# Kernel tuning notes

Hardware: AMD Instinct MI355X
Metric: run time of the kernel (lower is better)

The kernel has to match this reference:

```python
import jax, jax.numpy as jnp
import numpy as np

N_NODES = 100000
N_EDGES = 1600000
BN_EPS = 1e-5

def gin_layer(h, src, dst, eps, w1, b1, w2, b2, gamma, beta, mean, var):
    # message passing: sum of source-node features at each target node
    agg = jax.ops.segment_sum(h[src], dst, num_segments=h.shape[0])  # [N, H]
    z = (1.0 + eps) * h + agg
    z = jax.nn.relu(z @ w1 + b1)
    z = jax.nn.relu(z @ w2 + b2)
    # BatchNorm1d in eval mode (running stats as params)
    return gamma * (z - mean) * jax.lax.rsqrt(var + BN_EPS) + beta

def setup_inputs() -> dict:
    key = jax.random.key(0)
    ks = jax.random.split(key, 12)
    H = 64
    s = lambda fan: 1.0 / np.sqrt(fan)
    inp = {
        "x": jax.random.normal(ks[0], (N_NODES, 128), jnp.float32),
        "edge_index": jax.random.randint(ks[1], (2, N_EDGES), 0, N_NODES, jnp.int64),
        "eps": jnp.zeros((3,), jnp.float32),
        "c1_w1": jax.random.normal(ks[2], (128, H), jnp.float32) * s(128),
        "c1_b1": jnp.zeros((H,), jnp.float32),
        "c1_w2": jax.random.normal(ks[3], (H, H), jnp.float32) * s(H),
        "c1_b2": jnp.zeros((H,), jnp.float32),
        "c1_gamma": jnp.ones((H,), jnp.float32),
        "c1_beta": jnp.zeros((H,), jnp.float32),
        "c1_mean": jnp.zeros((H,), jnp.float32),
        "c1_var": jnp.ones((H,), jnp.float32),
        "cw1": jax.random.normal(ks[4], (2, H, H), jnp.float32) * s(H),
        "cb1": jnp.zeros((2, H), jnp.float32),
        "cw2": jax.random.normal(ks[5], (2, H, H), jnp.float32) * s(H),
        "cb2": jnp.zeros((2, H), jnp.float32),
        "cgamma": jnp.ones((2, H), jnp.float32),
        "cbeta": jnp.zeros((2, H), jnp.float32),
        "cmean": jnp.zeros((2, H), jnp.float32),
        "cvar": jnp.ones((2, H), jnp.float32),
        "lin1_w": jax.random.normal(ks[6], (H, H), jnp.float32) * s(H),
        "lin1_b": jnp.zeros((H,), jnp.float32),
        "lin2_w": jax.random.normal(ks[7], (H, 40), jnp.float32) * s(H),
        "lin2_b": jnp.zeros((40,), jnp.float32),
    }
    return inp

def reference(x, edge_index, eps, c1_w1, c1_b1, c1_w2, c1_b2, c1_gamma, c1_beta,
              c1_mean, c1_var, cw1, cb1, cw2, cb2, cgamma, cbeta, cmean, cvar,
              lin1_w, lin1_b, lin2_w, lin2_b):
    src, dst = edge_index[0], edge_index[1]
    h = gin_layer(x, src, dst, eps[0], c1_w1, c1_b1, c1_w2, c1_b2,
                  c1_gamma, c1_beta, c1_mean, c1_var)
    for i in range(2):  # num_layers - 1 stacked GINConvs
        h = gin_layer(h, src, dst, eps[i + 1], cw1[i], cb1[i], cw2[i], cb2[i],
                      cgamma[i], cbeta[i], cmean[i], cvar[i])
    h = jax.nn.relu(h @ lin1_w + lin1_b)
    # dropout(p=0.5) is identity in eval mode
    return h @ lin2_w + lin2_b  # logits [N, num_classes]
```

## Files before the change

kernel.cpp:

```cpp
#include <hip/hip_runtime.h>

#define NN 100000
#define NE 1600000
#define BN_EPS 1e-5f
#define NCOARSE 98
#define SC_CH 2048

typedef unsigned int u32;
typedef unsigned short u16;

static constexpr size_t OFF_ROW  = 0;
static constexpr size_t OFF_CTRL = 512u * 1024;
static constexpr size_t OFF_CSR  = 1u << 20;
static constexpr size_t OFF_U    = 8u << 20;
static constexpr size_t OFF_P1   = OFF_U;
static constexpr size_t OFF_YB0  = OFF_U + (size_t)NN * 64 * 4;
static constexpr size_t OFF_YB1  = OFF_YB0 + (size_t)NN * 64 * 2;

__device__ __forceinline__ u16 f2bf(float f) {
  u32 u = __float_as_uint(f);
  return (u16)((u + 0x7fffu + ((u >> 16) & 1u)) >> 16);
}
__device__ __forceinline__ float bflo(u32 u) { return __uint_as_float(u << 16); }
__device__ __forceinline__ float bfhi(u32 u) { return __uint_as_float(u & 0xffff0000u); }
__device__ __forceinline__ u32 pkbf(float lo, float hi) {
  return (u32)f2bf(lo) | ((u32)f2bf(hi) << 16);
}

typedef __bf16 bf16x8 __attribute__((ext_vector_type(8)));
typedef float f32x4 __attribute__((ext_vector_type(4)));
union FragCvt { uint4 u; bf16x8 b; u16 s[8]; };
__device__ __forceinline__ bf16x8 frag_u16(const u16* p) {
  FragCvt c; c.u = *(const uint4*)p; return c.b;
}

__global__ void __launch_bounds__(256) k_hist_c(const int* __restrict__ dst,
                                                int* __restrict__ ch) {
  __shared__ int h[NCOARSE];
  if (threadIdx.x < NCOARSE) h[threadIdx.x] = 0;
  __syncthreads();
  int i = blockIdx.x * 256 + threadIdx.x, stride = gridDim.x * 256;
  for (; i < NE; i += stride) atomicAdd(&h[dst[i] >> 10], 1);
  __syncthreads();
  if (threadIdx.x < NCOARSE && h[threadIdx.x]) atomicAdd(&ch[threadIdx.x], h[threadIdx.x]);
}

__global__ void __launch_bounds__(256) k_scat1(const int* __restrict__ src,
                                               const int* __restrict__ dst,
                                               const int* __restrict__ ch,
                                               int* __restrict__ reserve,
                                               u32* __restrict__ pairs1) {
  __shared__ int coffL[NCOARSE];
  __shared__ int h[NCOARSE], base[NCOARSE];
  int t = threadIdx.x;
  if (t < NCOARSE) { h[t] = 0; coffL[t] = ch[t]; }
  __syncthreads();
  if (t == 0) {
    int acc = 0;
    for (int i = 0; i < NCOARSE; i++) { int v = coffL[i]; coffL[i] = acc; acc += v; }
  }
  int e0 = blockIdx.x * SC_CH;
  int myc[8]; u32 mypk[8];
#pragma unroll
  for (int q = 0; q < 8; q++) {
    int e = e0 + q * 256 + t;
    if (e < NE) {
      int d = dst[e], s = src[e];
      myc[q] = d >> 10;
      mypk[q] = (u32)s | ((u32)(d & 1023) << 17);
      atomicAdd(&h[myc[q]], 1);
    } else myc[q] = -1;
  }
  __syncthreads();
  if (t < NCOARSE) {
    base[t] = (h[t] > 0) ? (coffL[t] + atomicAdd(&reserve[t], h[t])) : 0;
    h[t] = 0;
  }
  __syncthreads();
#pragma unroll
  for (int q = 0; q < 8; q++) {
    if (myc[q] >= 0) {
      int p = atomicAdd(&h[myc[q]], 1);
      pairs1[base[myc[q]] + p] = mypk[q];
    }
  }
}

__global__ void __launch_bounds__(256) k_fill3(const u32* __restrict__ pairs1,
                                               const int* __restrict__ ch,
                                               int* __restrict__ row,
                                               int* __restrict__ csr) {
  __shared__ int coffL[NCOARSE + 1];
  __shared__ int lcnt[1024];
  __shared__ int loff[1024];
  __shared__ int sd[256];
  __shared__ u32 stage[20480];
  int c = blockIdx.x, t = threadIdx.x;
  if (t < NCOARSE) coffL[t] = ch[t];
  __syncthreads();
  if (t == 0) {
    int acc = 0;
    for (int i = 0; i < NCOARSE; i++) { int v = coffL[i]; coffL[i] = acc; acc += v; }
    coffL[NCOARSE] = acc;
  }
  for (int i = t; i < 1024; i += 256) lcnt[i] = 0;
  __syncthreads();
  int es = coffL[c], ee = coffL[c + 1];
  int m = ee - es;
  int nbase = c << 10;
  int nodes_in = NN - nbase; if (nodes_in > 1024) nodes_in = 1024;
  for (int i = es + t; i < ee; i += 256)
    atomicAdd(&lcnt[(pairs1[i] >> 17) & 1023], 1);
  __syncthreads();
  int b4 = t * 4;
  int c0 = lcnt[b4], c1 = lcnt[b4 + 1], c2 = lcnt[b4 + 2], c3 = lcnt[b4 + 3];
  int s4 = c0 + c1 + c2 + c3;
  sd[t] = s4;
  __syncthreads();
  for (int o = 1; o < 256; o <<= 1) {
    int x = (t >= o) ? sd[t - o] : 0;
    __syncthreads();
    sd[t] += x;
    __syncthreads();
  }
  int run = sd[t] - s4;
  loff[b4] = run;     run += c0;
  loff[b4 + 1] = run; run += c1;
  loff[b4 + 2] = run; run += c2;
  loff[b4 + 3] = run;
  __syncthreads();
  for (int i = t; i < nodes_in; i += 256) row[nbase + i] = es + loff[i];
  if (c == NCOARSE - 1 && t == 0) row[NN] = NE;
  for (int i = t; i < 1024; i += 256) lcnt[i] = loff[i];
  __syncthreads();
  if (m <= 20480) {
    for (int i = es + t; i < ee; i += 256) {
      u32 pk = pairs1[i];
      int p = atomicAdd(&lcnt[(pk >> 17) & 1023], 1);
      stage[p] = pk & 0x1FFFFu;
    }
    __syncthreads();
    for (int i = t; i < m; i += 256) csr[es + i] = (int)stage[i];
  } else {
    for (int i = es + t; i < ee; i += 256) {
      u32 pk = pairs1[i];
      int p = atomicAdd(&lcnt[(pk >> 17) & 1023], 1);
      csr[es + p] = (int)(pk & 0x1FFFFu);
    }
  }
}

__global__ void __launch_bounds__(256) k_gemm_x_mfma(const float* __restrict__ x,
                                                     const float* __restrict__ w,
                                                     u16* __restrict__ yb) {
  __shared__ __align__(16) u16 wT[64][136];
  __shared__ __align__(16) u16 ht[4][32][72];
  int tid = threadIdx.x;
  for (int idx = tid; idx < 8192; idx += 256) {
    int k = idx >> 6, n = idx & 63;
    wT[n][k] = f2bf(w[idx]);
  }
  __syncthreads();
  int wid = tid >> 6, lane = tid & 63;
  int grp = blockIdx.x * 4 + wid;
  if (grp >= NN / 32) return;
  int g0 = grp * 32;
  int mrow = lane & 15;
  int kc8 = (lane >> 4) * 8;
  int q4 = (lane >> 4) * 4;
  bf16x8 a[2][4];
#pragma unroll
  for (int mt = 0; mt < 2; mt++) {
    const float* xr = x + (size_t)(g0 + mt * 16 + mrow) * 128;
#pragma unroll
    for (int kc = 0; kc < 4; kc++) {
      float4 v0 = *(const float4*)(xr + kc * 32 + kc8);
      float4 v1 = *(const float4*)(xr + kc * 32 + kc8 + 4);
      FragCvt fc;
      fc.s[0] = f2bf(v0.x); fc.s[1] = f2bf(v0.y); fc.s[2] = f2bf(v0.z); fc.s[3] = f2bf(v0.w);
      fc.s[4] = f2bf(v1.x); fc.s[5] = f2bf(v1.y); fc.s[6] = f2bf(v1.z); fc.s[7] = f2bf(v1.w);
      a[mt][kc] = fc.b;
    }
  }
  f32x4 zero = {0.f, 0.f, 0.f, 0.f};
  f32x4 acc[2][4];
#pragma unroll
  for (int nt = 0; nt < 4; nt++) {
    bf16x8 bf[4];
#pragma unroll
    for (int kc = 0; kc < 4; kc++)
      bf[kc] = frag_u16(&wT[nt * 16 + mrow][kc * 32 + kc8]);
#pragma unroll
    for (int mt = 0; mt < 2; mt++) {
      f32x4 c = __builtin_amdgcn_mfma_f32_16x16x32_bf16(a[mt][0], bf[0], zero, 0, 0, 0);
      c = __builtin_amdgcn_mfma_f32_16x16x32_bf16(a[mt][1], bf[1], c, 0, 0, 0);
      c = __builtin_amdgcn_mfma_f32_16x16x32_bf16(a[mt][2], bf[2], c, 0, 0, 0);
      c = __builtin_amdgcn_mfma_f32_16x16x32_bf16(a[mt][3], bf[3], c, 0, 0, 0);
      acc[mt][nt] = c;
    }
  }
#pragma unroll
  for (int mt = 0; mt < 2; mt++)
#pragma unroll
    for (int nt = 0; nt < 4; nt++)
#pragma unroll
      for (int r = 0; r < 4; r++)
        ht[wid][mt * 16 + q4 + r][nt * 16 + mrow] = f2bf(acc[mt][nt][r]);
  asm volatile("s_waitcnt lgkmcnt(0)" ::: "memory");
#pragma unroll
  for (int it = 0; it < 4; it++) {
    int idx = it * 64 + lane;
    int rw = idx >> 3, ch2 = idx & 7;
    uint4 v = *(const uint4*)&ht[wid][rw][ch2 * 8];
    *(uint4*)(yb + (size_t)(g0 + rw) * 64 + ch2 * 8) = v;
  }
}

__global__ void __launch_bounds__(256) k_agg(
    const u16* __restrict__ yb, const int* __restrict__ row, const int* __restrict__ csr,
    const float* __restrict__ epsv, int ei, const float* __restrict__ b1,
    u16* __restrict__ ub) {
  int t = blockIdx.x * 256 + threadIdx.x;
  int n = t >> 3, g = t & 7;
  if (n >= NN) return;
  const u16* bp = yb + g * 8;
  float a0 = 0, a1 = 0, a2 = 0, a3 = 0, a4 = 0, a5 = 0, a6 = 0, a7 = 0;
  int rs = row[n], re = row[n + 1];
  int i = rs;
  int headEnd = rs + ((4 - (rs & 3)) & 3);
  if (headEnd > re) headEnd = re;
  for (; i < headEnd; ++i) {
    int s = csr[i];
    uint4 v0 = *(const uint4*)(bp + (size_t)s * 64);
    a0 += bflo(v0.x); a1 += bfhi(v0.x); a2 += bflo(v0.y); a3 += bfhi(v0.y);
    a4 += bflo(v0.z); a5 += bfhi(v0.z); a6 += bflo(v0.w); a7 += bfhi(v0.w);
  }
  for (; i + 8 <= re; i += 8) {
    int4 c0 = *(const int4*)(csr + i);
    int4 c1 = *(const int4*)(csr + i + 4);
    int sidx[8] = {c0.x, c0.y, c0.z, c0.w, c1.x, c1.y, c1.z, c1.w};
    uint4 v[8];
#pragma unroll
    for (int q = 0; q < 8; q++)
      v[q] = *(const uint4*)(bp + (size_t)sidx[q] * 64);
#pragma unroll
    for (int q = 0; q < 8; q++) {
      a0 += bflo(v[q].x); a1 += bfhi(v[q].x); a2 += bflo(v[q].y); a3 += bfhi(v[q].y);
      a4 += bflo(v[q].z); a5 += bfhi(v[q].z); a6 += bflo(v[q].w); a7 += bfhi(v[q].w);
    }
  }
  if (i + 4 <= re) {
    int4 c0 = *(const int4*)(csr + i);
    int sidx[4] = {c0.x, c0.y, c0.z, c0.w};
    uint4 v[4];
#pragma unroll
    for (int q = 0; q < 4; q++)
      v[q] = *(const uint4*)(bp + (size_t)sidx[q] * 64);
#pragma unroll
    for (int q = 0; q < 4; q++) {
      a0 += bflo(v[q].x); a1 += bfhi(v[q].x); a2 += bflo(v[q].y); a3 += bfhi(v[q].y);
      a4 += bflo(v[q].z); a5 += bfhi(v[q].z); a6 += bflo(v[q].w); a7 += bfhi(v[q].w);
    }
    i += 4;
  }
  for (; i < re; ++i) {
    int s = csr[i];
    uint4 v0 = *(const uint4*)(bp + (size_t)s * 64);
    a0 += bflo(v0.x); a1 += bfhi(v0.x); a2 += bflo(v0.y); a3 += bfhi(v0.y);
    a4 += bflo(v0.z); a5 += bfhi(v0.z); a6 += bflo(v0.w); a7 += bfhi(v0.w);
  }
  uint4 sv = *(const uint4*)(bp + (size_t)n * 64);
  float e1 = 1.0f + epsv[ei];
  const float* bb = b1 + g * 8;
  float r0 = fmaxf(fmaf(e1, bflo(sv.x), a0 + bb[0]), 0.f);
  float r1 = fmaxf(fmaf(e1, bfhi(sv.x), a1 + bb[1]), 0.f);
  float r2 = fmaxf(fmaf(e1, bflo(sv.y), a2 + bb[2]), 0.f);
  float r3 = fmaxf(fmaf(e1, bfhi(sv.y), a3 + bb[3]), 0.f);
  float r4 = fmaxf(fmaf(e1, bflo(sv.z), a4 + bb[4]), 0.f);
  float r5 = fmaxf(fmaf(e1, bfhi(sv.z), a5 + bb[5]), 0.f);
  float r6 = fmaxf(fmaf(e1, bflo(sv.w), a6 + bb[6]), 0.f);
  float r7 = fmaxf(fmaf(e1, bfhi(sv.w), a7 + bb[7]), 0.f);
  uint4 pk;
  pk.x = pkbf(r0, r1); pk.y = pkbf(r2, r3);
  pk.z = pkbf(r4, r5); pk.w = pkbf(r6, r7);
  *(uint4*)(ub + (size_t)n * 64 + g * 8) = pk;
}

__global__ void __launch_bounds__(256) k_mlp_mfma(
    const u16* __restrict__ ub, const float* __restrict__ w2, const float* __restrict__ b2,
    const float* __restrict__ gamma, const float* __restrict__ beta,
    const float* __restrict__ mean, const float* __restrict__ var,
    const float* __restrict__ wn, u16* __restrict__ yout) {
  __shared__ __align__(16) u16 w2T[64][72];
  __shared__ __align__(16) u16 wnT[64][72];
  __shared__ __align__(16) u16 ht[4][32][72];
  int tid = threadIdx.x;
  for (int idx = tid; idx < 4096; idx += 256) {
    int k = idx >> 6, n = idx & 63;
    w2T[n][k] = f2bf(w2[idx]);
    wnT[n][k] = f2bf(wn[idx]);
  }
  __syncthreads();
  int wid = tid >> 6, lane = tid & 63;
  int grp = blockIdx.x * 4 + wid;
  if (grp >= NN / 32) return;
  int g0 = grp * 32;
  int mrow = lane & 15;
  int kc8 = (lane >> 4) * 8;
  int q4 = (lane >> 4) * 4;
  float bb[4], gl[4], be[4], mn[4], rv[4];
#pragma unroll
  for (int nt = 0; nt < 4; nt++) {
    int j = nt * 16 + mrow;
    bb[nt] = b2[j]; gl[nt] = gamma[j]; be[nt] = beta[j]; mn[nt] = mean[j];
    rv[nt] = rsqrtf(var[j] + BN_EPS);
  }
  bf16x8 a[2][2];
#pragma unroll
  for (int mt = 0; mt < 2; mt++)
#pragma unroll
    for (int kc = 0; kc < 2; kc++)
      a[mt][kc] = frag_u16(ub + (size_t)(g0 + mt * 16 + mrow) * 64 + kc * 32 + kc8);
  f32x4 zero = {0.f, 0.f, 0.f, 0.f};
  f32x4 acc[2][4];
#pragma unroll
  for (int nt = 0; nt < 4; nt++) {
    bf16x8 b0 = frag_u16(&w2T[nt * 16 + mrow][kc8]);
    bf16x8 b1f = frag_u16(&w2T[nt * 16 + mrow][32 + kc8]);
#pragma unroll
    for (int mt = 0; mt < 2; mt++) {
      acc[mt][nt] = __builtin_amdgcn_mfma_f32_16x16x32_bf16(a[mt][0], b0, zero, 0, 0, 0);
      acc[mt][nt] = __builtin_amdgcn_mfma_f32_16x16x32_bf16(a[mt][1], b1f, acc[mt][nt], 0, 0, 0);
    }
  }
#pragma unroll
  for (int mt = 0; mt < 2; mt++)
#pragma unroll
    for (int nt = 0; nt < 4; nt++)
#pragma unroll
      for (int r = 0; r < 4; r++) {
        float v = fmaxf(acc[mt][nt][r] + bb[nt], 0.f);
        float h = fmaf(gl[nt] * (v - mn[nt]), rv[nt], be[nt]);
        ht[wid][mt * 16 + q4 + r][nt * 16 + mrow] = f2bf(h);
      }
  asm volatile("s_waitcnt lgkmcnt(0)" ::: "memory");
  bf16x8 a2[2][2];
#pragma unroll
  for (int mt = 0; mt < 2; mt++)
#pragma unroll
    for (int kc = 0; kc < 2; kc++)
      a2[mt][kc] = frag_u16(&ht[wid][mt * 16 + mrow][kc * 32 + kc8]);
  f32x4 ac2[2][4];
#pragma unroll
  for (int nt = 0; nt < 4; nt++) {
    bf16x8 b0 = frag_u16(&wnT[nt * 16 + mrow][kc8]);
    bf16x8 b1f = frag_u16(&wnT[nt * 16 + mrow][32 + kc8]);
#pragma unroll
    for (int mt = 0; mt < 2; mt++) {
      ac2[mt][nt] = __builtin_amdgcn_mfma_f32_16x16x32_bf16(a2[mt][0], b0, zero, 0, 0, 0);
      ac2[mt][nt] = __builtin_amdgcn_mfma_f32_16x16x32_bf16(a2[mt][1], b1f, ac2[mt][nt], 0, 0, 0);
    }
  }
  asm volatile("s_waitcnt lgkmcnt(0)" ::: "memory");
#pragma unroll
  for (int mt = 0; mt < 2; mt++)
#pragma unroll
    for (int nt = 0; nt < 4; nt++)
#pragma unroll
      for (int r = 0; r < 4; r++)
        ht[wid][mt * 16 + q4 + r][nt * 16 + mrow] = f2bf(ac2[mt][nt][r]);
  asm volatile("s_waitcnt lgkmcnt(0)" ::: "memory");
#pragma unroll
  for (int it = 0; it < 4; it++) {
    int idx = it * 64 + lane;
    int rw = idx >> 3, ch2 = idx & 7;
    uint4 v = *(const uint4*)&ht[wid][rw][ch2 * 8];
    *(uint4*)(yout + (size_t)(g0 + rw) * 64 + ch2 * 8) = v;
  }
}

__global__ void __launch_bounds__(256) k_mlp_final_mfma(
    const u16* __restrict__ ub, const float* __restrict__ w2, const float* __restrict__ b2,
    const float* __restrict__ gamma, const float* __restrict__ beta,
    const float* __restrict__ mean, const float* __restrict__ var,
    const float* __restrict__ l1w, const float* __restrict__ l1b,
    const float* __restrict__ l2w, const float* __restrict__ l2b,
    float* __restrict__ out) {
  __shared__ __align__(16) u16 w2T[64][72];
  __shared__ __align__(16) u16 l1T[64][72];
  __shared__ __align__(16) u16 l2T[48][72];
  __shared__ __align__(16) u16 ht[4][32][72];
  int tid = threadIdx.x;
  for (int idx = tid; idx < 4096; idx += 256) {
    int k = idx >> 6, n = idx & 63;
    w2T[n][k] = f2bf(w2[idx]);
    l1T[n][k] = f2bf(l1w[idx]);
  }
  for (int idx = tid; idx < 3072; idx += 256) {
    int n = idx >> 6, k = idx & 63;
    l2T[n][k] = f2bf((n < 40) ? l2w[k * 40 + n] : 0.f);
  }
  __syncthreads();
  int wid = tid >> 6, lane = tid & 63;
  int grp = blockIdx.x * 4 + wid;
  if (grp >= NN / 32) return;
  int g0 = grp * 32;
  int mrow = lane & 15;
  int kc8 = (lane >> 4) * 8;
  int q4 = (lane >> 4) * 4;
  float bb[4], gl[4], be[4], mn[4], rv[4], l1bv[4];
#pragma unroll
  for (int nt = 0; nt < 4; nt++) {
    int j = nt * 16 + mrow;
    bb[nt] = b2[j]; gl[nt] = gamma[j]; be[nt] = beta[j]; mn[nt] = mean[j];
    rv[nt] = rsqrtf(var[j] + BN_EPS); l1bv[nt] = l1b[j];
  }
  float l2bv[3];
#pragma unroll
  for (int nt = 0; nt < 3; nt++) {
    int j = nt * 16 + mrow;
    l2bv[nt] = (j < 40) ? l2b[j] : 0.f;
  }
  bf16x8 a[2][2];
#pragma unroll
  for (int mt = 0; mt < 2; mt++)
#pragma unroll
    for (int kc = 0; kc < 2; kc++)
      a[mt][kc] = frag_u16(ub + (size_t)(g0 + mt * 16 + mrow) * 64 + kc * 32 + kc8);
  f32x4 zero = {0.f, 0.f, 0.f, 0.f};
  f32x4 acc[2][4];
#pragma unroll
  for (int nt = 0; nt < 4; nt++) {
    bf16x8 b0 = frag_u16(&w2T[nt * 16 + mrow][kc8]);
    bf16x8 b1f = frag_u16(&w2T[nt * 16 + mrow][32 + kc8]);
#pragma unroll
    for (int mt = 0; mt < 2; mt++) {
      acc[mt][nt] = __builtin_amdgcn_mfma_f32_16x16x32_bf16(a[mt][0], b0, zero, 0, 0, 0);
      acc[mt][nt] = __builtin_amdgcn_mfma_f32_16x16x32_bf16(a[mt][1], b1f, acc[mt][nt], 0, 0, 0);
    }
  }
#pragma unroll
  for (int mt = 0; mt < 2; mt++)
#pragma unroll
    for (int nt = 0; nt < 4; nt++)
#pragma unroll
      for (int r = 0; r < 4; r++) {
        float v = fmaxf(acc[mt][nt][r] + bb[nt], 0.f);
        float h = fmaf(gl[nt] * (v - mn[nt]), rv[nt], be[nt]);
        ht[wid][mt * 16 + q4 + r][nt * 16 + mrow] = f2bf(h);
      }
  asm volatile("s_waitcnt lgkmcnt(0)" ::: "memory");
  bf16x8 a2[2][2];
#pragma unroll
  for (int mt = 0; mt < 2; mt++)
#pragma unroll
    for (int kc = 0; kc < 2; kc++)
      a2[mt][kc] = frag_u16(&ht[wid][mt * 16 + mrow][kc * 32 + kc8]);
  f32x4 ac2[2][4];
#pragma unroll
  for (int nt = 0; nt < 4; nt++) {
    bf16x8 b0 = frag_u16(&l1T[nt * 16 + mrow][kc8]);
    bf16x8 b1f = frag_u16(&l1T[nt * 16 + mrow][32 + kc8]);
#pragma unroll
    for (int mt = 0; mt < 2; mt++) {
      ac2[mt][nt] = __builtin_amdgcn_mfma_f32_16x16x32_bf16(a2[mt][0], b0, zero, 0, 0, 0);
      ac2[mt][nt] = __builtin_amdgcn_mfma_f32_16x16x32_bf16(a2[mt][1], b1f, ac2[mt][nt], 0, 0, 0);
    }
  }
  asm volatile("s_waitcnt lgkmcnt(0)" ::: "memory");
#pragma unroll
  for (int mt = 0; mt < 2; mt++)
#pragma unroll
    for (int nt = 0; nt < 4; nt++)
#pragma unroll
      for (int r = 0; r < 4; r++) {
        float f = fmaxf(ac2[mt][nt][r] + l1bv[nt], 0.f);
        ht[wid][mt * 16 + q4 + r][nt * 16 + mrow] = f2bf(f);
      }
  asm volatile("s_waitcnt lgkmcnt(0)" ::: "memory");
  bf16x8 a3[2][2];
#pragma unroll
  for (int mt = 0; mt < 2; mt++)
#pragma unroll
    for (int kc = 0; kc < 2; kc++)
      a3[mt][kc] = frag_u16(&ht[wid][mt * 16 + mrow][kc * 32 + kc8]);
  f32x4 ac3[2][3];
#pragma unroll
  for (int nt = 0; nt < 3; nt++) {
    bf16x8 b0 = frag_u16(&l2T[nt * 16 + mrow][kc8]);
    bf16x8 b1f = frag_u16(&l2T[nt * 16 + mrow][32 + kc8]);
#pragma unroll
    for (int mt = 0; mt < 2; mt++) {
      ac3[mt][nt] = __builtin_amdgcn_mfma_f32_16x16x32_bf16(a3[mt][0], b0, zero, 0, 0, 0);
      ac3[mt][nt] = __builtin_amdgcn_mfma_f32_16x16x32_bf16(a3[mt][1], b1f, ac3[mt][nt], 0, 0, 0);
    }
  }
#pragma unroll
  for (int mt = 0; mt < 2; mt++)
#pragma unroll
    for (int nt = 0; nt < 3; nt++) {
      int j = nt * 16 + mrow;
      if (j < 40) {
#pragma unroll
        for (int r = 0; r < 4; r++)
          out[(size_t)(g0 + mt * 16 + q4 + r) * 40 + j] = ac3[mt][nt][r] + l2bv[nt];
      }
    }
}

extern "C" void kernel_launch(void* const* d_in, const int* in_sizes, int n_in,
                              void* d_out, int out_size, void* d_ws, size_t ws_size,
                              hipStream_t stream) {
  const float* x   = (const float*)d_in[0];
  const int*   ei  = (const int*)d_in[1];
  const int*   src = ei;
  const int*   dst = ei + NE;
  const float* eps = (const float*)d_in[2];
  const float* c1_w1 = (const float*)d_in[3];
  const float* c1_b1 = (const float*)d_in[4];
  const float* c1_w2 = (const float*)d_in[5];
  const float* c1_b2 = (const float*)d_in[6];
  const float* c1_gamma = (const float*)d_in[7];
  const float* c1_beta  = (const float*)d_in[8];
  const float* c1_mean  = (const float*)d_in[9];
  const float* c1_var   = (const float*)d_in[10];
  const float* cw1 = (const float*)d_in[11];
  const float* cb1 = (const float*)d_in[12];
  const float* cw2 = (const float*)d_in[13];
  const float* cb2 = (const float*)d_in[14];
  const float* cgamma = (const float*)d_in[15];
  const float* cbeta  = (const float*)d_in[16];
  const float* cmean  = (const float*)d_in[17];
  const float* cvar   = (const float*)d_in[18];
  const float* lin1_w = (const float*)d_in[19];
  const float* lin1_b = (const float*)d_in[20];
  const float* lin2_w = (const float*)d_in[21];
  const float* lin2_b = (const float*)d_in[22];
  float* out = (float*)d_out;

  char* ws = (char*)d_ws;
  int* row  = (int*)(ws + OFF_ROW);
  int* ctrl = (int*)(ws + OFF_CTRL);
  int* ch      = ctrl;
  int* reserve = ctrl + 128;
  int* csr  = (int*)(ws + OFF_CSR);
  u32* pairs1 = (u32*)(ws + OFF_P1);
  u16* ubuf = (u16*)(ws + OFF_U);
  u16* yb0  = (u16*)(ws + OFF_YB0);
  u16* yb1  = (u16*)(ws + OFF_YB1);

  hipMemsetAsync(ctrl, 0, 256 * 4, stream);

  k_hist_c<<<512, 256, 0, stream>>>(dst, ch);
  k_scat1<<<(NE + SC_CH - 1) / SC_CH, 256, 0, stream>>>(src, dst, ch, reserve, pairs1);
  k_fill3<<<NCOARSE, 256, 0, stream>>>(pairs1, ch, row, csr);

  const int AGG_GRID = (NN * 8) / 256;
  const int MLP_GRID = (NN / 32 + 3) / 4;

  k_gemm_x_mfma<<<MLP_GRID, 256, 0, stream>>>(x, c1_w1, yb0);

  k_agg<<<AGG_GRID, 256, 0, stream>>>(yb0, row, csr, eps, 0, c1_b1, ubuf);
  k_mlp_mfma<<<MLP_GRID, 256, 0, stream>>>(ubuf, c1_w2, c1_b2,
                                           c1_gamma, c1_beta, c1_mean, c1_var,
                                           cw1, yb1);
  k_agg<<<AGG_GRID, 256, 0, stream>>>(yb1, row, csr, eps, 1, cb1, ubuf);
  k_mlp_mfma<<<MLP_GRID, 256, 0, stream>>>(ubuf, cw2, cb2,
                                           cgamma, cbeta, cmean, cvar,
                                           cw1 + 64 * 64, yb0);
  k_agg<<<AGG_GRID, 256, 0, stream>>>(yb0, row, csr, eps, 2, cb1 + 64, ubuf);
  k_mlp_final_mfma<<<MLP_GRID, 256, 0, stream>>>(ubuf, cw2 + 64 * 64, cb2 + 64,
                                                 cgamma + 64, cbeta + 64, cmean + 64, cvar + 64,
                                                 lin1_w, lin1_b, lin2_w, lin2_b,
                                                 out);
}
```

Before: 235.9 us.

## Quantize gathered node features to int8 with per-row scales for aggregation

The GEMM epilogues now quantize each 64-wide output row to int8 with a per-row absmax scale instead of storing bf16. The aggregation kernel gathers the 8-byte int8 chunks plus a float scale per neighbor and dequantizes with FMAs. This halves the bytes moved by the random neighbor gather, which dominates the message-passing kernels. In exchange it adds a scale load per edge, drops the vectorized CSR index loads and the alignment head loop, and loses precision, which may break tolerance checks.

```diff
diff --git a/kernel.cpp b/kernel.cpp
--- a/kernel.cpp
+++ b/kernel.cpp
@@ -8,14 +8,17 @@
 
 typedef unsigned int u32;
 typedef unsigned short u16;
+typedef signed char s8;
 
 static constexpr size_t OFF_ROW  = 0;
 static constexpr size_t OFF_CTRL = 512u * 1024;
 static constexpr size_t OFF_CSR  = 1u << 20;
 static constexpr size_t OFF_U    = 8u << 20;
 static constexpr size_t OFF_P1   = OFF_U;
-static constexpr size_t OFF_YB0  = OFF_U + (size_t)NN * 64 * 4;
-static constexpr size_t OFF_YB1  = OFF_YB0 + (size_t)NN * 64 * 2;
+static constexpr size_t OFF_Q0   = 22u << 20;
+static constexpr size_t OFF_S0   = 30u << 20;
+static constexpr size_t OFF_Q1   = 32u << 20;
+static constexpr size_t OFF_S1   = 40u << 20;
 
 __device__ __forceinline__ u16 f2bf(float f) {
   u32 u = __float_as_uint(f);
@@ -32,6 +35,27 @@
 union FragCvt { uint4 u; bf16x8 b; u16 s[8]; };
 __device__ __forceinline__ bf16x8 frag_u16(const u16* p) {
   FragCvt c; c.u = *(const uint4*)p; return c.b;
+}
+
+__device__ __forceinline__ uint2 q8(uint4 hv, float inv) {
+  float v0 = bflo(hv.x), v1 = bfhi(hv.x), v2 = bflo(hv.y), v3 = bfhi(hv.y);
+  float v4 = bflo(hv.z), v5 = bfhi(hv.z), v6 = bflo(hv.w), v7 = bfhi(hv.w);
+  int q0 = (int)rintf(v0 * inv), q1 = (int)rintf(v1 * inv);
+  int q2 = (int)rintf(v2 * inv), q3 = (int)rintf(v3 * inv);
+  int q4 = (int)rintf(v4 * inv), q5 = (int)rintf(v5 * inv);
+  int q6 = (int)rintf(v6 * inv), q7 = (int)rintf(v7 * inv);
+  uint2 r;
+  r.x = (u32)(q0 & 0xff) | ((u32)(q1 & 0xff) << 8) | ((u32)(q2 & 0xff) << 16) | ((u32)(q3 & 0xff) << 24);
+  r.y = (u32)(q4 & 0xff) | ((u32)(q5 & 0xff) << 8) | ((u32)(q6 & 0xff) << 16) | ((u32)(q7 & 0xff) << 24);
+  return r;
+}
+__device__ __forceinline__ float habs8(uint4 hv) {
+  float m = fabsf(bflo(hv.x));
+  m = fmaxf(m, fabsf(bfhi(hv.x))); m = fmaxf(m, fabsf(bflo(hv.y)));
+  m = fmaxf(m, fabsf(bfhi(hv.y))); m = fmaxf(m, fabsf(bflo(hv.z)));
+  m = fmaxf(m, fabsf(bfhi(hv.z))); m = fmaxf(m, fabsf(bflo(hv.w)));
+  m = fmaxf(m, fabsf(bfhi(hv.w)));
+  return m;
 }
 
 __global__ void __launch_bounds__(256) k_hist_c(const int* __restrict__ dst,
@@ -152,7 +176,8 @@
 
 __global__ void __launch_bounds__(256) k_gemm_x_mfma(const float* __restrict__ x,
                                                      const float* __restrict__ w,
-                                                     u16* __restrict__ yb) {
+                                                     s8* __restrict__ qt,
+                                                     float* __restrict__ scal) {
   __shared__ __align__(16) u16 wT[64][136];
   __shared__ __align__(16) u16 ht[4][32][72];
   int tid = threadIdx.x;
@@ -211,75 +236,93 @@
   for (int it = 0; it < 4; it++) {
     int idx = it * 64 + lane;
     int rw = idx >> 3, ch2 = idx & 7;
-    uint4 v = *(const uint4*)&ht[wid][rw][ch2 * 8];
-    *(uint4*)(yb + (size_t)(g0 + rw) * 64 + ch2 * 8) = v;
+    uint4 hv = *(const uint4*)&ht[wid][rw][ch2 * 8];
+    float m = habs8(hv);
+    m = fmaxf(m, __shfl_xor(m, 1));
+    m = fmaxf(m, __shfl_xor(m, 2));
+    m = fmaxf(m, __shfl_xor(m, 4));
+    float inv = (m > 0.f) ? 127.0f / m : 0.f;
+    uint2 qv = q8(hv, inv);
+    *(uint2*)(qt + (size_t)(g0 + rw) * 64 + ch2 * 8) = qv;
+    if (ch2 == 0) scal[g0 + rw] = m * (1.0f / 127.0f);
   }
 }
 
 __global__ void __launch_bounds__(256) k_agg(
-    const u16* __restrict__ yb, const int* __restrict__ row, const int* __restrict__ csr,
+    const s8* __restrict__ qt, const float* __restrict__ scal,
+    const int* __restrict__ row, const int* __restrict__ csr,
     const float* __restrict__ epsv, int ei, const float* __restrict__ b1,
     u16* __restrict__ ub) {
   int t = blockIdx.x * 256 + threadIdx.x;
   int n = t >> 3, g = t & 7;
   if (n >= NN) return;
-  const u16* bp = yb + g * 8;
+  const s8* bp = qt + g * 8;
   float a0 = 0, a1 = 0, a2 = 0, a3 = 0, a4 = 0, a5 = 0, a6 = 0, a7 = 0;
   int rs = row[n], re = row[n + 1];
   int i = rs;
-  int headEnd = rs + ((4 - (rs & 3)) & 3);
-  if (headEnd > re) headEnd = re;
-  for (; i < headEnd; ++i) {
-    int s = csr[i];
-    uint4 v0 = *(const uint4*)(bp + (size_t)s * 64);
-    a0 += bflo(v0.x); a1 += bfhi(v0.x); a2 += bflo(v0.y); a3 += bfhi(v0.y);
-    a4 += bflo(v0.z); a5 += bfhi(v0.z); a6 += bflo(v0.w); a7 += bfhi(v0.w);
-  }
+#define DQ8(qv, sc) { \
+    a0 = fmaf(sc, (float)(int)(s8)((qv).x), a0); \
+    a1 = fmaf(sc, (float)(int)(s8)((qv).x >> 8), a1); \
+    a2 = fmaf(sc, (float)(int)(s8)((qv).x >> 16), a2); \
+    a3 = fmaf(sc, (float)(int)(s8)((qv).x >> 24), a3); \
+    a4 = fmaf(sc, (float)(int)(s8)((qv).y), a4); \
+    a5 = fmaf(sc, (float)(int)(s8)((qv).y >> 8), a5); \
+    a6 = fmaf(sc, (float)(int)(s8)((qv).y >> 16), a6); \
+    a7 = fmaf(sc, (float)(int)(s8)((qv).y >> 24), a7); }
   for (; i + 8 <= re; i += 8) {
-    int4 c0 = *(const int4*)(csr + i);
-    int4 c1 = *(const int4*)(csr + i + 4);
-    int sidx[8] = {c0.x, c0.y, c0.z, c0.w, c1.x, c1.y, c1.z, c1.w};
-    uint4 v[8];
-#pragma unroll
-    for (int q = 0; q < 8; q++)
-      v[q] = *(const uint4*)(bp + (size_t)sidx[q] * 64);
+    int sidx[8];
+#pragma unroll
+    for (int q = 0; q < 8; q++) sidx[q] = csr[i + q];
+    uint2 v[8]; float sc[8];
 #pragma unroll
     for (int q = 0; q < 8; q++) {
-      a0 += bflo(v[q].x); a1 += bfhi(v[q].x); a2 += bflo(v[q].y); a3 += bfhi(v[q].y);
-      a4 += bflo(v[q].z); a5 += bfhi(v[q].z); a6 += bflo(v[q].w); a7 += bfhi(v[q].w);
-    }
+      v[q] = *(const uint2*)(bp + (size_t)sidx[q] * 64);
+      sc[q] = scal[sidx[q]];
+    }
+#pragma unroll
+    for (int q = 0; q < 8; q++) DQ8(v[q], sc[q]);
   }
   if (i + 4 <= re) {
-    int4 c0 = *(const int4*)(csr + i);
-    int sidx[4] = {c0.x, c0.y, c0.z, c0.w};
-    uint4 v[4];
-#pragma unroll
-    for (int q = 0; q < 4; q++)
-      v[q] = *(const uint4*)(bp + (size_t)sidx[q] * 64);
+    int sidx[4];
+#pragma unroll
+    for (int q = 0; q < 4; q++) sidx[q] = csr[i + q];
+    uint2 v[4]; float sc[4];
 #pragma unroll
     for (int q = 0; q < 4; q++) {
-      a0 += bflo(v[q].x); a1 += bfhi(v[q].x); a2 += bflo(v[q].y); a3 += bfhi(v[q].y);
-      a4 += bflo(v[q].z); a5 += bfhi(v[q].z); a6 += bflo(v[q].w); a7 += bfhi(v[q].w);
-    }
+      v[q] = *(const uint2*)(bp + (size_t)sidx[q] * 64);
+      sc[q] = scal[sidx[q]];
+    }
+#pragma unroll
+    for (int q = 0; q < 4; q++) DQ8(v[q], sc[q]);
     i += 4;
   }
   for (; i < re; ++i) {
     int s = csr[i];
-    uint4 v0 = *(const uint4*)(bp + (size_t)s * 64);
-    a0 += bflo(v0.x); a1 += bfhi(v0.x); a2 += bflo(v0.y); a3 += bfhi(v0.y);
-    a4 += bflo(v0.z); a5 += bfhi(v0.z); a6 += bflo(v0.w); a7 += bfhi(v0.w);
-  }
-  uint4 sv = *(const uint4*)(bp + (size_t)n * 64);
+    uint2 v0 = *(const uint2*)(bp + (size_t)s * 64);
+    float sc = scal[s];
+    DQ8(v0, sc);
+  }
+#undef DQ8
+  uint2 sv = *(const uint2*)(bp + (size_t)n * 64);
+  float ssc = scal[n];
+  float s0 = ssc * (float)(int)(s8)(sv.x);
+  float s1 = ssc * (float)(int)(s8)(sv.x >> 8);
+  float s2 = ssc * (float)(int)(s8)(sv.x >> 16);
+  float s3 = ssc * (float)(int)(s8)(sv.x >> 24);
+  float s4 = ssc * (float)(int)(s8)(sv.y);
+  float s5 = ssc * (float)(int)(s8)(sv.y >> 8);
+  float s6 = ssc * (float)(int)(s8)(sv.y >> 16);
+  float s7 = ssc * (float)(int)(s8)(sv.y >> 24);
   float e1 = 1.0f + epsv[ei];
   const float* bb = b1 + g * 8;
-  float r0 = fmaxf(fmaf(e1, bflo(sv.x), a0 + bb[0]), 0.f);
-  float r1 = fmaxf(fmaf(e1, bfhi(sv.x), a1 + bb[1]), 0.f);
-  float r2 = fmaxf(fmaf(e1, bflo(sv.y), a2 + bb[2]), 0.f);
-  float r3 = fmaxf(fmaf(e1, bfhi(sv.y), a3 + bb[3]), 0.f);
-  float r4 = fmaxf(fmaf(e1, bflo(sv.z), a4 + bb[4]), 0.f);
-  float r5 = fmaxf(fmaf(e1, bfhi(sv.z), a5 + bb[5]), 0.f);
-  float r6 = fmaxf(fmaf(e1, bflo(sv.w), a6 + bb[6]), 0.f);
-  float r7 = fmaxf(fmaf(e1, bfhi(sv.w), a7 + bb[7]), 0.f);
+  float r0 = fmaxf(fmaf(e1, s0, a0 + bb[0]), 0.f);
+  float r1 = fmaxf(fmaf(e1, s1, a1 + bb[1]), 0.f);
+  float r2 = fmaxf(fmaf(e1, s2, a2 + bb[2]), 0.f);
+  float r3 = fmaxf(fmaf(e1, s3, a3 + bb[3]), 0.f);
+  float r4 = fmaxf(fmaf(e1, s4, a4 + bb[4]), 0.f);
+  float r5 = fmaxf(fmaf(e1, s5, a5 + bb[5]), 0.f);
+  float r6 = fmaxf(fmaf(e1, s6, a6 + bb[6]), 0.f);
+  float r7 = fmaxf(fmaf(e1, s7, a7 + bb[7]), 0.f);
   uint4 pk;
   pk.x = pkbf(r0, r1); pk.y = pkbf(r2, r3);
   pk.z = pkbf(r4, r5); pk.w = pkbf(r6, r7);
@@ -290,7 +333,7 @@
     const u16* __restrict__ ub, const float* __restrict__ w2, const float* __restrict__ b2,
     const float* __restrict__ gamma, const float* __restrict__ beta,
     const float* __restrict__ mean, const float* __restrict__ var,
-    const float* __restrict__ wn, u16* __restrict__ yout) {
+    const float* __restrict__ wn, s8* __restrict__ qt, float* __restrict__ scal) {
   __shared__ __align__(16) u16 w2T[64][72];
   __shared__ __align__(16) u16 wnT[64][72];
   __shared__ __align__(16) u16 ht[4][32][72];
@@ -374,8 +417,15 @@
   for (int it = 0; it < 4; it++) {
     int idx = it * 64 + lane;
     int rw = idx >> 3, ch2 = idx & 7;
-    uint4 v = *(const uint4*)&ht[wid][rw][ch2 * 8];
-    *(uint4*)(yout + (size_t)(g0 + rw) * 64 + ch2 * 8) = v;
+    uint4 hv = *(const uint4*)&ht[wid][rw][ch2 * 8];
+    float m = habs8(hv);
+    m = fmaxf(m, __shfl_xor(m, 1));
+    m = fmaxf(m, __shfl_xor(m, 2));
+    m = fmaxf(m, __shfl_xor(m, 4));
+    float inv = (m > 0.f) ? 127.0f / m : 0.f;
+    uint2 qv = q8(hv, inv);
+    *(uint2*)(qt + (size_t)(g0 + rw) * 64 + ch2 * 8) = qv;
+    if (ch2 == 0) scal[g0 + rw] = m * (1.0f / 127.0f);
   }
 }
 
@@ -546,8 +596,10 @@
   int* csr  = (int*)(ws + OFF_CSR);
   u32* pairs1 = (u32*)(ws + OFF_P1);
   u16* ubuf = (u16*)(ws + OFF_U);
-  u16* yb0  = (u16*)(ws + OFF_YB0);
-  u16* yb1  = (u16*)(ws + OFF_YB1);
+  s8*  q0   = (s8*)(ws + OFF_Q0);
+  float* s0 = (float*)(ws + OFF_S0);
+  s8*  q1   = (s8*)(ws + OFF_Q1);
+  float* s1 = (float*)(ws + OFF_S1);
 
   hipMemsetAsync(ctrl, 0, 256 * 4, stream);
 
@@ -558,17 +610,17 @@
   const int AGG_GRID = (NN * 8) / 256;
   const int MLP_GRID = (NN / 32 + 3) / 4;
 
-  k_gemm_x_mfma<<<MLP_GRID, 256, 0, stream>>>(x, c1_w1, yb0);
-
-  k_agg<<<AGG_GRID, 256, 0, stream>>>(yb0, row, csr, eps, 0, c1_b1, ubuf);
+  k_gemm_x_mfma<<<MLP_GRID, 256, 0, stream>>>(x, c1_w1, q0, s0);
+
+  k_agg<<<AGG_GRID, 256, 0, stream>>>(q0, s0, row, csr, eps, 0, c1_b1, ubuf);
   k_mlp_mfma<<<MLP_GRID, 256, 0, stream>>>(ubuf, c1_w2, c1_b2,
                                            c1_gamma, c1_beta, c1_mean, c1_var,
-                                           cw1, yb1);
-  k_agg<<<AGG_GRID, 256, 0, stream>>>(yb1, row, csr, eps, 1, cb1, ubuf);
+                                           cw1, q1, s1);
+  k_agg<<<AGG_GRID, 256, 0, stream>>>(q1, s1, row, csr, eps, 1, cb1, ubuf);
   k_mlp_mfma<<<MLP_GRID, 256, 0, stream>>>(ubuf, cw2, cb2,
                                            cgamma, cbeta, cmean, cvar,
-                                           cw1 + 64 * 64, yb0);
-  k_agg<<<AGG_GRID, 256, 0, stream>>>(yb0, row, csr, eps, 2, cb1 + 64, ubuf);
+                                           cw1 + 64 * 64, q0, s0);
+  k_agg<<<AGG_GRID, 256, 0, stream>>>(q0, s0, row, csr, eps, 2, cb1 + 64, ubuf);
   k_mlp_final_mfma<<<MLP_GRID, 256, 0, stream>>>(ubuf, cw2 + 64 * 64, cb2 + 64,
                                                  cgamma + 64, cbeta + 64, cmean + 64, cvar + 64,
                                                  lin1_w, lin1_b, lin2_w, lin2_b,
```

Result: no change. 232.3 us (-1.6%).
